# Kernel tuning notes

Measured on AMD Instinct MI355X. Metric: run time of the kernel, lower is better.

## Reference

```python
import jax, jax.numpy as jnp
import numpy as np

N_NODES = 50000
N_FEAT = 128
N_EDGES = 800000
HEADS1 = 4
HID1 = 64
HID2 = 128
N_CLASSES = 10
N_GRAPHS = 512
NEG_SLOPE_ATT = 0.2   # GATConv attention leaky relu
NEG_SLOPE_ACT = 0.01  # F.leaky_relu default between layers


def setup_inputs() -> dict:
    key = jax.random.key(0)
    ks = jax.random.split(key, 20)
    s = 0.05
    inp = {
        'x': jax.random.normal(ks[0], (N_NODES, N_FEAT), dtype=jnp.float32),
        'edge_index': jax.random.randint(ks[1], (2, N_EDGES), 0, N_NODES, dtype=jnp.int64),
        'edge_attr': jax.random.normal(ks[2], (N_EDGES, 8), dtype=jnp.float32),
        'batch': jnp.sort(jax.random.randint(ks[3], (N_NODES,), 0, N_GRAPHS, dtype=jnp.int64)),
        # conv1: F -> HID1, heads=4, concat
        'W1': jax.random.normal(ks[4], (N_FEAT, HEADS1 * HID1), dtype=jnp.float32) * s,
        'a_src1': jax.random.normal(ks[5], (HEADS1, HID1), dtype=jnp.float32) * s,
        'a_dst1': jax.random.normal(ks[6], (HEADS1, HID1), dtype=jnp.float32) * s,
        'b1': jnp.zeros((HEADS1 * HID1,), dtype=jnp.float32),
        # conv2: 4*HID1 -> HID2, heads=1
        'W2': jax.random.normal(ks[7], (HEADS1 * HID1, HID2), dtype=jnp.float32) * s,
        'a_src2': jax.random.normal(ks[8], (1, HID2), dtype=jnp.float32) * s,
        'a_dst2': jax.random.normal(ks[9], (1, HID2), dtype=jnp.float32) * s,
        'b2': jnp.zeros((HID2,), dtype=jnp.float32),
        # conv3: HID2 -> N_CLASSES, heads=1
        'W3': jax.random.normal(ks[10], (HID2, N_CLASSES), dtype=jnp.float32) * s,
        'a_src3': jax.random.normal(ks[11], (1, N_CLASSES), dtype=jnp.float32) * s,
        'a_dst3': jax.random.normal(ks[12], (1, N_CLASSES), dtype=jnp.float32) * s,
        'b3': jnp.zeros((N_CLASSES,), dtype=jnp.float32),
    }
    return inp


def gat_conv(x, src, dst, W, a_src, a_dst, b, n_nodes, heads, ch):
    """PyG GATConv (concat=True, add_self_loops already applied in src/dst)."""
    h = (x @ W).reshape(n_nodes, heads, ch)            # [N,H,C]
    al_s = (h * a_src).sum(-1)                          # [N,H]
    al_d = (h * a_dst).sum(-1)                          # [N,H]
    e = jax.nn.leaky_relu(al_s[src] + al_d[dst], NEG_SLOPE_ATT)  # [E,H]
    # segment softmax over incoming edges per destination node
    m = jax.ops.segment_max(e, dst, num_segments=n_nodes)
    ex = jnp.exp(e - m[dst])
    den = jax.ops.segment_sum(ex, dst, num_segments=n_nodes)
    alpha = ex / (den[dst] + 1e-16)                     # [E,H]
    out = jax.ops.segment_sum(h[src] * alpha[..., None], dst, num_segments=n_nodes)
    return out.reshape(n_nodes, heads * ch) + b


def reference(x, edge_index, edge_attr, batch,
              W1, a_src1, a_dst1, b1,
              W2, a_src2, a_dst2, b2,
              W3, a_src3, a_dst3, b3):
    # GATConv adds self-loops by default; edge_attr unused (edge_dim=None)
    loops = jnp.arange(N_NODES, dtype=edge_index.dtype)
    src = jnp.concatenate([edge_index[0], loops])
    dst = jnp.concatenate([edge_index[1], loops])

    h = gat_conv(x, src, dst, W1, a_src1, a_dst1, b1, N_NODES, HEADS1, HID1)
    h = jax.nn.leaky_relu(h, NEG_SLOPE_ACT)
    h = gat_conv(h, src, dst, W2, a_src2, a_dst2, b2, N_NODES, 1, HID2)
    h = jax.nn.leaky_relu(h, NEG_SLOPE_ACT)
    h = gat_conv(h, src, dst, W3, a_src3, a_dst3, b3, N_NODES, 1, N_CLASSES)

    pooled = jax.ops.segment_sum(h, batch, num_segments=N_GRAPHS)  # global_add_pool
    return jax.nn.log_softmax(pooled, axis=1), pooled
```

## Files before the change

kernel.cpp:

```cpp
#include <hip/hip_runtime.h>
#include <math.h>

#define NNODES 50000
#define MPAD   50048
#define NFEAT  128
#define NEDGE  800000
#define ETOT   (NEDGE + NNODES)
#define H1     4
#define O1     256
#define C2     128
#define C3     10
#define NGRAPH 512

#define NBKT   196
#define NBLK1  831
#define EPB    1024
#define SCM    (NBKT * NBLK1)
#define SCB    637

typedef __attribute__((ext_vector_type(8))) short short8;
typedef __attribute__((ext_vector_type(4))) float f32x4;
typedef __attribute__((ext_vector_type(2))) float f32x2;

__device__ __forceinline__ unsigned short f2b(float f) {
  unsigned int u = __float_as_uint(f);
  u += 0x7fffu + ((u >> 16) & 1u);
  return (unsigned short)(u >> 16);
}
__device__ __forceinline__ float b2f(unsigned short u) {
  return __uint_as_float(((unsigned int)u) << 16);
}
__device__ __forceinline__ float readlane_f(float v, int l) {
  return __uint_as_float((unsigned)__builtin_amdgcn_readlane(__float_as_uint(v), l));
}


__global__ void k_prep(const float* __restrict__ W1, const float* __restrict__ as1,
                       const float* __restrict__ ad1,
                       float* __restrict__ was, float* __restrict__ wad) {
  int tid = threadIdx.x;
  int h = tid >> 7, k = tid & 127;
  float s = 0.f, d = 0.f;
  for (int j = 0; j < 64; ++j) {
    float w = W1[(size_t)k * 256 + h * 64 + j];
    s += w * as1[h * 64 + j];
    d += w * ad1[h * 64 + j];
  }
  was[h * 128 + k] = s;
  wad[h * 128 + k] = d;
}

#define NB_CVT 12500

__global__ __launch_bounds__(256) void k_front(
    const int* __restrict__ src_e, const int* __restrict__ dst_e,
    int* __restrict__ hists,
    const float* __restrict__ X, unsigned short* __restrict__ Xb,
    const float* __restrict__ W1,
    const float* __restrict__ was, const float* __restrict__ wad,
    float* __restrict__ als, float* __restrict__ ald,
    unsigned short* __restrict__ W1p,
    const float* __restrict__ W2, unsigned short* __restrict__ W2p,
    const float* __restrict__ W3, unsigned short* __restrict__ W3p) {
  const int b = blockIdx.x;
  const int tid = threadIdx.x;
  if (b < NBLK1) {
    __shared__ int h[NBKT];
    if (tid < NBKT) h[tid] = 0;
    __syncthreads();
    const int base = b * EPB;
#pragma unroll
    for (int r = 0; r < 4; ++r) {
      int e = base + r * 256 + tid;
      if (e < ETOT) {
        int d = (e < NEDGE) ? dst_e[e] : (e - NEDGE);
        atomicAdd(&h[d >> 8], 1);
      }
    }
    __syncthreads();
    if (tid < NBKT) hists[tid * NBLK1 + b] = h[tid];
  } else if (b < NBLK1 + NB_CVT) {
    const int n = (b - NBLK1) * 4 + (tid >> 6);
    const int lane = tid & 63;
    const int k0 = lane * 2;
    float2 xv = *(const float2*)(X + (size_t)n * 128 + k0);
    ushort2 o; o.x = f2b(xv.x); o.y = f2b(xv.y);
    *(ushort2*)(Xb + (size_t)n * 128 + k0) = o;
    float s[4], d[4];
#pragma unroll
    for (int h = 0; h < 4; ++h) {
      float2 wsv = *(const float2*)(was + h * 128 + k0);
      float2 wdv = *(const float2*)(wad + h * 128 + k0);
      s[h] = xv.x * wsv.x + xv.y * wsv.y;
      d[h] = xv.x * wdv.x + xv.y * wdv.y;
    }
#pragma unroll
    for (int m = 1; m < 64; m <<= 1)
#pragma unroll
      for (int h = 0; h < 4; ++h) { s[h] += __shfl_xor(s[h], m); d[h] += __shfl_xor(d[h], m); }
    if (lane == 0) {
#pragma unroll
      for (int h = 0; h < 4; ++h) {
        als[(size_t)n * 4 + h] = s[h];
        ald[(size_t)n * 4 + h] = d[h];
      }
    }
  } else if (b < NBLK1 + NB_CVT + 128) {
    int idx = (b - NBLK1 - NB_CVT) * 256 + tid;
    int h = idx >> 13, r = idx & 8191;
    int j = r & 7, lane = (r >> 3) & 63, t = r >> 9;
    int ks = t & 3, nt = t >> 2;
    int k = ks * 32 + (lane >> 4) * 8 + j;
    int n = nt * 16 + (lane & 15);
    W1p[idx] = f2b(W1[(size_t)k * 256 + h * 64 + n]);
  } else if (b < NBLK1 + NB_CVT + 256) {
    int idx = (b - NBLK1 - NB_CVT - 128) * 256 + tid;
    int j = idx & 7, lane = (idx >> 3) & 63, t = idx >> 9;
    int ks = t % 8, nt = t / 8;
    int k = ks * 32 + (lane >> 4) * 8 + j;
    int n = nt * 16 + (lane & 15);
    W2p[idx] = f2b(W2[(size_t)k * C2 + n]);
  } else {
    int idx = (b - NBLK1 - NB_CVT - 256) * 256 + tid;
    int j = idx & 7, lane = (idx >> 3) & 63, t = idx >> 9;
    int ks = t & 3, nt = t >> 2;
    int k = ks * 32 + (lane >> 4) * 8 + j;
    int n = nt * 16 + (lane & 15);
    W3p[idx] = f2b((n < C3) ? W3[(size_t)k * C3 + n] : 0.f);
  }
}


__global__ __launch_bounds__(256) void k_scanA2(const int* __restrict__ a,
                                                int* __restrict__ bsum) {
  int idx = blockIdx.x * 256 + threadIdx.x;
  int v = (idx < SCM) ? a[idx] : 0;
#pragma unroll
  for (int m = 1; m < 64; m <<= 1) v += __shfl_xor(v, m);
  __shared__ int ws[4];
  int lane = threadIdx.x & 63, wid = threadIdx.x >> 6;
  if (lane == 0) ws[wid] = v;
  __syncthreads();
  if (threadIdx.x == 0) bsum[blockIdx.x] = ws[0] + ws[1] + ws[2] + ws[3];
}

__global__ __launch_bounds__(256) void k_scanMid(int* __restrict__ bsum) {
  __shared__ int ws[4];
  __shared__ int carry_s;
  const int tid = threadIdx.x, lane = tid & 63, wid = tid >> 6;
  if (tid == 0) carry_s = 0;
  __syncthreads();
  for (int base = 0; base < SCB; base += 256) {
    int j = base + tid;
    int v = (j < SCB) ? bsum[j] : 0;
    int s = v;
#pragma unroll
    for (int m = 1; m < 64; m <<= 1) {
      int t = __shfl_up(s, m);
      if (lane >= m) s += t;
    }
    if (lane == 63) ws[wid] = s;
    __syncthreads();
    int woff = 0;
#pragma unroll
    for (int k = 0; k < 4; ++k)
      if (k < wid) woff += ws[k];
    int c = carry_s;
    int tot = ws[0] + ws[1] + ws[2] + ws[3];
    if (j < SCB) bsum[j] = c + woff + s - v;
    __syncthreads();
    if (tid == 0) carry_s = c + tot;
    __syncthreads();
  }
}

__global__ __launch_bounds__(256) void k_scanB2(int* __restrict__ a,
                                                const int* __restrict__ bsum,
                                                int* __restrict__ cb) {
  const int b = blockIdx.x, tid = threadIdx.x;
  const int lane = tid & 63, wid = tid >> 6;
  __shared__ int ws[4];
  int idx = b * 256 + tid;
  int v = (idx < SCM) ? a[idx] : 0;
  int s = v;
#pragma unroll
  for (int m = 1; m < 64; m <<= 1) {
    int t = __shfl_up(s, m);
    if (lane >= m) s += t;
  }
  if (lane == 63) ws[wid] = s;
  __syncthreads();
  int woff = 0;
#pragma unroll
  for (int k = 0; k < 4; ++k)
    if (k < wid) woff += ws[k];
  int excl = bsum[b] + woff + s - v;
  if (idx < SCM) {
    a[idx] = excl;
    if (idx % NBLK1 == 0) cb[idx / NBLK1] = excl;
  }
  if (b == 0 && tid == 0) cb[NBKT] = ETOT;
}


__global__ __launch_bounds__(256) void k_part1(const int* __restrict__ src_e,
                                               const int* __restrict__ dst_e,
                                               const int* __restrict__ offs,
                                               unsigned* __restrict__ coarse) {
  __shared__ int cur[NBKT];
  const int b = blockIdx.x;
  const int tid = threadIdx.x;
  if (tid < NBKT) cur[tid] = offs[tid * NBLK1 + b];
  __syncthreads();
  const int base = b * EPB;
#pragma unroll
  for (int r = 0; r < 4; ++r) {
    int e = base + r * 256 + tid;
    if (e < ETOT) {
      int d, s;
      if (e < NEDGE) { d = dst_e[e]; s = src_e[e]; }
      else           { d = e - NEDGE; s = e - NEDGE; }
      int pos = atomicAdd(&cur[d >> 8], 1);
      coarse[pos] = ((unsigned)d << 16) | (unsigned)s;
    }
  }
}


__global__ __launch_bounds__(256) void k_bucket(const unsigned* __restrict__ coarse,
                                                const int* __restrict__ cb,
                                                int* __restrict__ rowptr,
                                                int* __restrict__ srcs) {
  const int b = blockIdx.x;
  const int tid = threadIdx.x;
  const int lane = tid & 63, wid = tid >> 6;
  const int lo = cb[b], hi = cb[b + 1];
  __shared__ int h[256];
  __shared__ int cur[256];
  __shared__ int ws[4];
  h[tid] = 0;
  __syncthreads();
  for (int i = lo + tid; i < hi; i += 256)
    atomicAdd(&h[(coarse[i] >> 16) & 255], 1);
  __syncthreads();
  int v = h[tid];
  int s = v;
#pragma unroll
  for (int m = 1; m < 64; m <<= 1) {
    int t = __shfl_up(s, m);
    if (lane >= m) s += t;
  }
  if (lane == 63) ws[wid] = s;
  __syncthreads();
  int woff = 0;
#pragma unroll
  for (int k = 0; k < 4; ++k)
    if (k < wid) woff += ws[k];
  int ex = woff + s - v;
  cur[tid] = lo + ex;
  int d = b * 256 + tid;
  if (d < NNODES) rowptr[d] = lo + ex;
  if (b == NBKT - 1 && tid == 0) rowptr[NNODES] = ETOT;
  __syncthreads();
  for (int i = lo + tid; i < hi; i += 256) {
    unsigned c = coarse[i];
    int pos = atomicAdd(&cur[(c >> 16) & 255], 1);
    srcs[pos] = (int)(c & 0xffffu);
  }
}


__global__ __launch_bounds__(512) void k_aggP(const int* __restrict__ rowptr,
                                              const int* __restrict__ srcs,
                                              const unsigned short* __restrict__ Xb,
                                              const float* __restrict__ als,
                                              const float* __restrict__ ald,
                                              unsigned short* __restrict__ P) {
  __shared__ float exs[8][16][4];
  const int wv = threadIdx.x >> 6;
  const int n = blockIdx.x * 8 + wv;
  const int lane = threadIdx.x & 63;
  const int r0 = rowptr[n], r1 = rowptr[n + 1];
  const int e_lane = lane & 15, hh = lane >> 4;
  const float aldv = ald[(size_t)n * 4 + hh];
  const int ch0 = lane * 2;
  f32x2 ah0 = {0.f, 0.f}, ah1 = {0.f, 0.f}, ah2 = {0.f, 0.f}, ah3 = {0.f, 0.f};
  float den = 0.f;
  for (int i0 = r0; i0 < r1; i0 += 16) {
    const int take = r1 - i0;
    int sidx = srcs[min(i0 + e_lane, r1 - 1)];
    float ev = als[(size_t)sidx * 4 + hh] + aldv;
    ev = (ev > 0.f) ? ev : 0.2f * ev;
    float exv = (e_lane < take) ? __expf(ev) : 0.f;
    den += exv;
    exs[wv][e_lane][hh] = exv;
    unsigned hv[16];
#pragma unroll
    for (int m = 0; m < 16; ++m) {
      int s = __builtin_amdgcn_readlane(sidx, m);
      hv[m] = *(const unsigned*)(Xb + (size_t)s * 128 + ch0);
    }
#pragma unroll
    for (int m = 0; m < 16; ++m) {
      f32x2 e01 = *(const f32x2*)(&exs[wv][m][0]);
      f32x2 e23 = *(const f32x2*)(&exs[wv][m][2]);
      f32x2 x2;
      x2.x = __uint_as_float(hv[m] << 16);
      x2.y = __uint_as_float(hv[m] & 0xffff0000u);
      asm("v_pk_fma_f32 %0, %1, %2, %0 op_sel:[0,0,0] op_sel_hi:[1,0,1]"
          : "+v"(ah0) : "v"(x2), "v"(e01));
      asm("v_pk_fma_f32 %0, %1, %2, %0 op_sel:[0,1,0] op_sel_hi:[1,1,1]"
          : "+v"(ah1) : "v"(x2), "v"(e01));
      asm("v_pk_fma_f32 %0, %1, %2, %0 op_sel:[0,0,0] op_sel_hi:[1,0,1]"
          : "+v"(ah2) : "v"(x2), "v"(e23));
      asm("v_pk_fma_f32 %0, %1, %2, %0 op_sel:[0,1,0] op_sel_hi:[1,1,1]"
          : "+v"(ah3) : "v"(x2), "v"(e23));
    }
  }
#pragma unroll
  for (int m = 1; m < 16; m <<= 1) den += __shfl_xor(den, m);
  float acc[4][2] = {{ah0.x, ah0.y}, {ah1.x, ah1.y}, {ah2.x, ah2.y}, {ah3.x, ah3.y}};
#pragma unroll
  for (int h = 0; h < 4; ++h) {
    float rd = 1.f / (readlane_f(den, h * 16) + 1e-16f);
    ushort2 o; o.x = f2b(acc[h][0] * rd); o.y = f2b(acc[h][1] * rd);
    *(ushort2*)(P + ((size_t)n * 4 + h) * 128 + ch0) = o;
  }
}


__global__ __launch_bounds__(256) void k_mmh(const unsigned short* __restrict__ P,
                                             const unsigned short* __restrict__ Wp,
                                             const float* __restrict__ b1,
                                             unsigned short* __restrict__ act1) {
  const int hy = blockIdx.y;
  const int w = threadIdx.x >> 6, lane = threadIdx.x & 63;
  const int arow = blockIdx.x * 64 + w * 16 + (lane & 15);
  const int k0 = (lane >> 4) * 8;
  const unsigned short* Ab = P + ((size_t)arow * 4 + hy) * 128;
  f32x4 acc[4] = {};
#pragma unroll
  for (int ks = 0; ks < 4; ++ks) {
    short8 a = *(const short8*)(Ab + ks * 32 + k0);
    const short8* bp = (const short8*)(Wp + (size_t)hy * 8192) + ks * 64 + lane;
#pragma unroll
    for (int nt = 0; nt < 4; ++nt) {
      short8 b = bp[(size_t)nt * 4 * 64];
      acc[nt] = __builtin_amdgcn_mfma_f32_16x16x32_bf16(a, b, acc[nt], 0, 0, 0);
    }
  }
  const int col = lane & 15;
  const int rbase = blockIdx.x * 64 + w * 16 + (lane >> 4) * 4;
#pragma unroll
  for (int nt = 0; nt < 4; ++nt) {
    int ch = hy * 64 + nt * 16 + col;
    float bb = b1[ch];
#pragma unroll
    for (int j = 0; j < 4; ++j) {
      float v = acc[nt][j] + bb;
      v = (v > 0.f) ? v : 0.01f * v;
      act1[(size_t)(rbase + j) * 256 + ch] = f2b(v);
    }
  }
}


template<int K, int N, int HEADS, int CREAL>
__global__ __launch_bounds__(256) void k_mm(const unsigned short* __restrict__ Xb,
                                            const unsigned short* __restrict__ Wp,
                                            unsigned short* __restrict__ Hout,
                                            const float* __restrict__ a_src,
                                            const float* __restrict__ a_dst,
                                            float* __restrict__ als,
                                            float* __restrict__ ald) {
  constexpr int KS = K / 32, NT = N / 16;
  constexpr int NTH = (NT + HEADS - 1) / HEADS;
  const int w = threadIdx.x >> 6, lane = threadIdx.x & 63;
  const int arow = blockIdx.x * 64 + w * 16 + (lane & 15);
  const int k0 = (lane >> 4) * 8;
  f32x4 acc[NT] = {};
  for (int ks = 0; ks < KS; ++ks) {
    short8 a = *(const short8*)(Xb + (size_t)arow * K + ks * 32 + k0);
    const short8* bp = (const short8*)Wp + (size_t)ks * 64 + lane;
#pragma unroll
    for (int nt = 0; nt < NT; ++nt) {
      short8 b = bp[(size_t)nt * KS * 64];
      acc[nt] = __builtin_amdgcn_mfma_f32_16x16x32_bf16(a, b, acc[nt], 0, 0, 0);
    }
  }
  const int col = lane & 15;
  const int rbase = blockIdx.x * 64 + w * 16 + (lane >> 4) * 4;
#pragma unroll
  for (int nt = 0; nt < NT; ++nt)
#pragma unroll
    for (int j = 0; j < 4; ++j)
      Hout[(size_t)(rbase + j) * N + nt * 16 + col] = f2b(acc[nt][j]);

  float av[NT], dv[NT];
#pragma unroll
  for (int nt = 0; nt < NT; ++nt) {
    int ch = nt * 16 + col;
    av[nt] = (ch < CREAL) ? a_src[ch] : 0.f;
    dv[nt] = (ch < CREAL) ? a_dst[ch] : 0.f;
  }
  float sa[HEADS][4], da[HEADS][4];
#pragma unroll
  for (int h = 0; h < HEADS; ++h)
#pragma unroll
    for (int j = 0; j < 4; ++j) { sa[h][j] = 0.f; da[h][j] = 0.f; }
#pragma unroll
  for (int nt = 0; nt < NT; ++nt) {
    int h = nt / NTH;
#pragma unroll
    for (int j = 0; j < 4; ++j) {
      sa[h][j] += acc[nt][j] * av[nt];
      da[h][j] += acc[nt][j] * dv[nt];
    }
  }
#pragma unroll
  for (int mask = 1; mask < 16; mask <<= 1)
#pragma unroll
    for (int h = 0; h < HEADS; ++h)
#pragma unroll
      for (int j = 0; j < 4; ++j) {
        sa[h][j] += __shfl_xor(sa[h][j], mask);
        da[h][j] += __shfl_xor(da[h][j], mask);
      }
  if (col == 0) {
#pragma unroll
    for (int j = 0; j < 4; ++j)
#pragma unroll
      for (int h = 0; h < HEADS; ++h) {
        als[(size_t)(rbase + j) * HEADS + h] = sa[h][j];
        ald[(size_t)(rbase + j) * HEADS + h] = da[h][j];
      }
  }
}


template<int C, bool ACT>
__global__ __launch_bounds__(512) void k_agg(const int* __restrict__ rowptr,
                                             const int* __restrict__ srcs,
                                             const unsigned short* __restrict__ Hm,
                                             const float* __restrict__ als,
                                             const float* __restrict__ ald,
                                             const float* __restrict__ bias,
                                             unsigned short* __restrict__ outb) {
  __shared__ float exs2[8][16];
  const int wv = threadIdx.x >> 6;
  const int n = blockIdx.x * 8 + wv;
  const int lane = threadIdx.x & 63;
  const int r0 = rowptr[n], r1 = rowptr[n + 1];
  const int e_lane = lane & 15;
  const int ch0 = lane * 2;
  const float aldm = ald[n];
  f32x2 accP0 = {0.f, 0.f}, accP1 = {0.f, 0.f};
  float den = 0.f;
  for (int i0 = r0; i0 < r1; i0 += 16) {
    const int take = r1 - i0;
    int sidx = srcs[min(i0 + e_lane, r1 - 1)];
    float ev = als[sidx] + aldm;
    ev = (ev > 0.f) ? ev : 0.2f * ev;
    float exv = (lane < 16 && e_lane < take) ? __expf(ev) : 0.f;
    den += exv;
    if (lane < 16) exs2[wv][lane] = exv;
    unsigned hv[16];
#pragma unroll
    for (int m = 0; m < 16; ++m) {
      int s = __builtin_amdgcn_readlane(sidx, m);
      hv[m] = *(const unsigned*)(Hm + (size_t)s * C + ch0);
    }
#pragma unroll
    for (int m = 0; m < 16; m += 2) {
      f32x2 ep = *(const f32x2*)(&exs2[wv][m]);
      f32x2 xa, xb;
      xa.x = __uint_as_float(hv[m] << 16);
      xa.y = __uint_as_float(hv[m + 1] << 16);
      xb.x = __uint_as_float(hv[m] & 0xffff0000u);
      xb.y = __uint_as_float(hv[m + 1] & 0xffff0000u);
      asm("v_pk_fma_f32 %0, %1, %2, %0" : "+v"(accP0) : "v"(ep), "v"(xa));
      asm("v_pk_fma_f32 %0, %1, %2, %0" : "+v"(accP1) : "v"(ep), "v"(xb));
    }
  }
#pragma unroll
  for (int mask = 1; mask < 64; mask <<= 1) den += __shfl_xor(den, mask);
  float acc0 = accP0.x + accP0.y;
  float acc1 = accP1.x + accP1.y;
  float rden = 1.f / (den + 1e-16f);
  float v0 = acc0 * rden + bias[ch0];
  float v1 = acc1 * rden + bias[ch0 + 1];
  if (ACT) { v0 = (v0 > 0.f) ? v0 : 0.01f * v0; v1 = (v1 > 0.f) ? v1 : 0.01f * v1; }
  ushort2 o; o.x = f2b(v0); o.y = f2b(v1);
  *(ushort2*)(outb + (size_t)n * C + ch0) = o;
}


__global__ __launch_bounds__(512) void k_agg3(const int* __restrict__ rowptr,
                                              const int* __restrict__ srcs,
                                              const unsigned short* __restrict__ Hm,
                                              const float* __restrict__ als,
                                              const float* __restrict__ ald,
                                              const float* __restrict__ bias,
                                              float* __restrict__ pooled,
                                              const int* __restrict__ batch) {
  __shared__ int   sid_s[8][4][16];
  __shared__ float exv_s[8][4][16];
  const int wv = threadIdx.x >> 6;
  const int lane = threadIdx.x & 63;
  const int g = lane >> 4, el = lane & 15;
  const int n = blockIdx.x * 32 + wv * 4 + g;
  const bool valid = n < NNODES;
  int r0 = 0, r1 = 0;
  float aldm = 0.f;
  if (valid) { r0 = rowptr[n]; r1 = rowptr[n + 1]; aldm = ald[n]; }
  float acc = 0.f, den = 0.f;
  for (int i0 = r0; i0 < r1; i0 += 16) {
    const int take = r1 - i0;
    int sidx = srcs[min(i0 + el, r1 - 1)];
    float ev = als[sidx] + aldm;
    ev = (ev > 0.f) ? ev : 0.2f * ev;
    float exv = (el < take) ? __expf(ev) : 0.f;
    den += exv;
    sid_s[wv][g][el] = sidx;
    exv_s[wv][g][el] = exv;
#pragma unroll
    for (int m = 0; m < 16; ++m) {
      int s = sid_s[wv][g][m];
      float ex = exv_s[wv][g][m];
      acc += ex * b2f(Hm[(size_t)s * 16 + el]);
    }
  }
#pragma unroll
  for (int mask = 1; mask < 16; mask <<= 1) den += __shfl_xor(den, mask);
  if (valid && el < C3) {
    float val = acc / (den + 1e-16f) + bias[el];
    atomicAdd(&pooled[(size_t)batch[n] * C3 + el], val);
  }
}


__global__ void k_lsm(const float* __restrict__ pooled, float* __restrict__ dout) {
  int g = blockIdx.x * 256 + threadIdx.x;
  if (g >= NGRAPH) return;
  float v[C3];
  float mx = -1e30f;
#pragma unroll
  for (int c = 0; c < C3; ++c) { v[c] = pooled[g * C3 + c]; mx = fmaxf(mx, v[c]); }
  float ssum = 0.f;
#pragma unroll
  for (int c = 0; c < C3; ++c) ssum += __expf(v[c] - mx);
  float lse = mx + __logf(ssum);
#pragma unroll
  for (int c = 0; c < C3; ++c) {
    dout[g * C3 + c] = v[c] - lse;
    dout[NGRAPH * C3 + g * C3 + c] = v[c];
  }
}


extern "C" void kernel_launch(void* const* d_in, const int* in_sizes, int n_in,
                              void* d_out, int out_size, void* d_ws, size_t ws_size,
                              hipStream_t stream) {
  (void)in_sizes; (void)n_in; (void)out_size; (void)ws_size;
  const float* x     = (const float*)d_in[0];
  const int*   eix   = (const int*)d_in[1];
  const int*   batch = (const int*)d_in[3];
  const float* W1 = (const float*)d_in[4];
  const float* as1 = (const float*)d_in[5];
  const float* ad1 = (const float*)d_in[6];
  const float* b1 = (const float*)d_in[7];
  const float* W2 = (const float*)d_in[8];
  const float* as2 = (const float*)d_in[9];
  const float* ad2 = (const float*)d_in[10];
  const float* b2 = (const float*)d_in[11];
  const float* W3 = (const float*)d_in[12];
  const float* as3 = (const float*)d_in[13];
  const float* ad3 = (const float*)d_in[14];
  const float* b3 = (const float*)d_in[15];
  const int* src_e = eix;
  const int* dst_e = eix + NEDGE;

  char* ws = (char*)d_ws;
  size_t off = 0;
  auto carve = [&](size_t bytes) -> char* {
    char* p = ws + off;
    off += (bytes + 511) & ~(size_t)511;
    return p;
  };
  int* hists  = (int*)carve((size_t)SCM * 4);
  int* bsum   = (int*)carve((size_t)SCB * 4);
  int* cb     = (int*)carve((size_t)(NBKT + 1) * 4);
  unsigned* coarse = (unsigned*)carve((size_t)ETOT * 4);
  int* rowptr = (int*)carve((size_t)(NNODES + 1) * 4);
  int* srcs   = (int*)carve((size_t)ETOT * 4);
  float* als  = (float*)carve((size_t)MPAD * H1 * 4);
  float* ald  = (float*)carve((size_t)MPAD * H1 * 4);
  float* was  = (float*)carve((size_t)512 * 4);
  float* wad  = (float*)carve((size_t)512 * 4);
  unsigned short* Xb   = (unsigned short*)carve((size_t)MPAD * 128 * 2);
  unsigned short* P    = (unsigned short*)carve((size_t)MPAD * 512 * 2);
  unsigned short* act1 = (unsigned short*)carve((size_t)MPAD * 256 * 2);
  unsigned short* Hb   = (unsigned short*)carve((size_t)MPAD * 128 * 2);
  unsigned short* Xc   = (unsigned short*)carve((size_t)MPAD * 128 * 2);
  unsigned short* H3b  = (unsigned short*)carve((size_t)MPAD * 16 * 2);
  float* pooled = (float*)carve((size_t)NGRAPH * C3 * 4);
  unsigned short* W1p = (unsigned short*)carve((size_t)4 * 8192 * 2);
  unsigned short* W2p = (unsigned short*)carve((size_t)O1 * C2 * 2);
  unsigned short* W3p = (unsigned short*)carve((size_t)C2 * 16 * 2);

  hipMemsetAsync(pooled, 0, (size_t)NGRAPH * C3 * 4, stream);

  k_prep<<<1, 512, 0, stream>>>(W1, as1, ad1, was, wad);
  k_front<<<NBLK1 + NB_CVT + 264, 256, 0, stream>>>(
      src_e, dst_e, hists, x, Xb, W1, was, wad, als, ald, W1p, W2, W2p, W3, W3p);
  k_scanA2<<<SCB, 256, 0, stream>>>(hists, bsum);
  k_scanMid<<<1, 256, 0, stream>>>(bsum);
  k_scanB2<<<SCB, 256, 0, stream>>>(hists, bsum, cb);
  k_part1<<<NBLK1, 256, 0, stream>>>(src_e, dst_e, hists, coarse);
  k_bucket<<<NBKT, 256, 0, stream>>>(coarse, cb, rowptr, srcs);

  const int GB = MPAD / 64;
  const int NB8 = NNODES / 8;
  const int NB32 = (NNODES + 31) / 32;

  k_aggP<<<NB8, 512, 0, stream>>>(rowptr, srcs, Xb, als, ald, P);
  k_mmh<<<dim3(GB, 4), 256, 0, stream>>>(P, W1p, b1, act1);

  k_mm<O1, C2, 1, C2><<<GB, 256, 0, stream>>>(act1, W2p, Hb, as2, ad2, als, ald);
  k_agg<C2, true><<<NB8, 512, 0, stream>>>(rowptr, srcs, Hb, als, ald, b2, Xc);

  k_mm<C2, 16, 1, C3><<<GB, 256, 0, stream>>>(Xc, W3p, H3b, as3, ad3, als, ald);
  k_agg3<<<NB32, 512, 0, stream>>>(rowptr, srcs, H3b, als, ald, b3, pooled, batch);

  k_lsm<<<(NGRAPH + 255) / 256, 256, 0, stream>>>(pooled, (float*)d_out);
}
```

Measured before the change: 226.4 us.

## Fuse layer-1 head matmul into aggP and layer-3 matmul into layer-2 aggregation

Layer-1 aggregation now keeps the per-node aggregated head features in shared memory and runs the per-head projection with MFMA inside the same block. This removes the large P intermediate buffer and the separate k_mmh launch. Layer-2 aggregation likewise stages its activated output in LDS and computes the conv3 projection and attention logits in one wave, so the Xc buffer and a k_mm launch go away. The cost is extra block-wide syncs, MFMA tiles that are half wasted (8 of 16 rows valid), and idle waves during the fused matmul.

```diff
diff --git a/kernel.cpp b/kernel.cpp
--- a/kernel.cpp
+++ b/kernel.cpp
@@ -275,8 +275,11 @@
                                               const unsigned short* __restrict__ Xb,
                                               const float* __restrict__ als,
                                               const float* __restrict__ ald,
-                                              unsigned short* __restrict__ P) {
+                                              const unsigned short* __restrict__ W1p,
+                                              const float* __restrict__ b1,
+                                              unsigned short* __restrict__ act1) {
   __shared__ float exs[8][16][4];
+  __shared__ unsigned short Pl[8][4][128];
   const int wv = threadIdx.x >> 6;
   const int n = blockIdx.x * 8 + wv;
   const int lane = threadIdx.x & 63;
@@ -324,42 +327,36 @@
   for (int h = 0; h < 4; ++h) {
     float rd = 1.f / (readlane_f(den, h * 16) + 1e-16f);
     ushort2 o; o.x = f2b(acc[h][0] * rd); o.y = f2b(acc[h][1] * rd);
-    *(ushort2*)(P + ((size_t)n * 4 + h) * 128 + ch0) = o;
-  }
-}
-
-
-__global__ __launch_bounds__(256) void k_mmh(const unsigned short* __restrict__ P,
-                                             const unsigned short* __restrict__ Wp,
-                                             const float* __restrict__ b1,
-                                             unsigned short* __restrict__ act1) {
-  const int hy = blockIdx.y;
-  const int w = threadIdx.x >> 6, lane = threadIdx.x & 63;
-  const int arow = blockIdx.x * 64 + w * 16 + (lane & 15);
+    *(ushort2*)(&Pl[wv][h][ch0]) = o;
+  }
+  __syncthreads();
+
+  const int row = lane & 15;
   const int k0 = (lane >> 4) * 8;
-  const unsigned short* Ab = P + ((size_t)arow * 4 + hy) * 128;
-  f32x4 acc[4] = {};
-#pragma unroll
-  for (int ks = 0; ks < 4; ++ks) {
-    short8 a = *(const short8*)(Ab + ks * 32 + k0);
-    const short8* bp = (const short8*)(Wp + (size_t)hy * 8192) + ks * 64 + lane;
-#pragma unroll
-    for (int nt = 0; nt < 4; ++nt) {
-      short8 b = bp[(size_t)nt * 4 * 64];
-      acc[nt] = __builtin_amdgcn_mfma_f32_16x16x32_bf16(a, b, acc[nt], 0, 0, 0);
-    }
-  }
   const int col = lane & 15;
-  const int rbase = blockIdx.x * 64 + w * 16 + (lane >> 4) * 4;
-#pragma unroll
-  for (int nt = 0; nt < 4; ++nt) {
-    int ch = hy * 64 + nt * 16 + col;
-    float bb = b1[ch];
+  const int rb = (lane >> 4) * 4;
+#pragma unroll
+  for (int u = 0; u < 2; ++u) {
+    const int unit = wv + 8 * u;
+    const int h = unit >> 2, nt = unit & 3;
+    f32x4 acc2 = {};
+#pragma unroll
+    for (int ks = 0; ks < 4; ++ks) {
+      short8 a{};
+      if (row < 8) a = *(const short8*)(&Pl[row][h][ks * 32 + k0]);
+      short8 b = *((const short8*)(W1p + (size_t)h * 8192) + nt * 256 + ks * 64 + lane);
+      acc2 = __builtin_amdgcn_mfma_f32_16x16x32_bf16(a, b, acc2, 0, 0, 0);
+    }
+    const int ch = h * 64 + nt * 16 + col;
+    const float bb = b1[ch];
 #pragma unroll
     for (int j = 0; j < 4; ++j) {
-      float v = acc[nt][j] + bb;
-      v = (v > 0.f) ? v : 0.01f * v;
-      act1[(size_t)(rbase + j) * 256 + ch] = f2b(v);
+      int r = rb + j;
+      if (r < 8) {
+        float v = acc2[j] + bb;
+        v = (v > 0.f) ? v : 0.01f * v;
+        act1[(size_t)(blockIdx.x * 8 + r) * 256 + ch] = f2b(v);
+      }
     }
   }
 }
@@ -438,15 +435,20 @@
 }
 
 
-template<int C, bool ACT>
-__global__ __launch_bounds__(512) void k_agg(const int* __restrict__ rowptr,
-                                             const int* __restrict__ srcs,
-                                             const unsigned short* __restrict__ Hm,
-                                             const float* __restrict__ als,
-                                             const float* __restrict__ ald,
-                                             const float* __restrict__ bias,
-                                             unsigned short* __restrict__ outb) {
+__global__ __launch_bounds__(512) void k_agg2(const int* __restrict__ rowptr,
+                                              const int* __restrict__ srcs,
+                                              const unsigned short* __restrict__ Hm,
+                                              const float* __restrict__ als,
+                                              const float* __restrict__ ald,
+                                              const float* __restrict__ bias,
+                                              const unsigned short* __restrict__ W3p,
+                                              const float* __restrict__ as3,
+                                              const float* __restrict__ ad3,
+                                              unsigned short* __restrict__ H3b,
+                                              float* __restrict__ als3,
+                                              float* __restrict__ ald3) {
   __shared__ float exs2[8][16];
+  __shared__ unsigned short Xl[8][128];
   const int wv = threadIdx.x >> 6;
   const int n = blockIdx.x * 8 + wv;
   const int lane = threadIdx.x & 63;
@@ -468,7 +470,7 @@
 #pragma unroll
     for (int m = 0; m < 16; ++m) {
       int s = __builtin_amdgcn_readlane(sidx, m);
-      hv[m] = *(const unsigned*)(Hm + (size_t)s * C + ch0);
+      hv[m] = *(const unsigned*)(Hm + (size_t)s * C2 + ch0);
     }
 #pragma unroll
     for (int m = 0; m < 16; m += 2) {
@@ -484,14 +486,47 @@
   }
 #pragma unroll
   for (int mask = 1; mask < 64; mask <<= 1) den += __shfl_xor(den, mask);
-  float acc0 = accP0.x + accP0.y;
-  float acc1 = accP1.x + accP1.y;
   float rden = 1.f / (den + 1e-16f);
-  float v0 = acc0 * rden + bias[ch0];
-  float v1 = acc1 * rden + bias[ch0 + 1];
-  if (ACT) { v0 = (v0 > 0.f) ? v0 : 0.01f * v0; v1 = (v1 > 0.f) ? v1 : 0.01f * v1; }
+  float v0 = (accP0.x + accP0.y) * rden + bias[ch0];
+  float v1 = (accP1.x + accP1.y) * rden + bias[ch0 + 1];
+  v0 = (v0 > 0.f) ? v0 : 0.01f * v0;
+  v1 = (v1 > 0.f) ? v1 : 0.01f * v1;
   ushort2 o; o.x = f2b(v0); o.y = f2b(v1);
-  *(ushort2*)(outb + (size_t)n * C + ch0) = o;
+  *(ushort2*)(&Xl[wv][ch0]) = o;
+  __syncthreads();
+
+  if (wv == 0) {
+    const int row = lane & 15;
+    const int k0 = (lane >> 4) * 8;
+    const int col = lane & 15;
+    f32x4 acc2 = {};
+#pragma unroll
+    for (int ks = 0; ks < 4; ++ks) {
+      short8 a{};
+      if (row < 8) a = *(const short8*)(&Xl[row][ks * 32 + k0]);
+      short8 b = *((const short8*)W3p + ks * 64 + lane);
+      acc2 = __builtin_amdgcn_mfma_f32_16x16x32_bf16(a, b, acc2, 0, 0, 0);
+    }
+    const float av = (col < C3) ? as3[col] : 0.f;
+    const float dv = (col < C3) ? ad3[col] : 0.f;
+    const int rb = (lane >> 4) * 4;
+#pragma unroll
+    for (int j = 0; j < 4; ++j) {
+      float hv = acc2[j];
+      float sa = hv * av, da = hv * dv;
+#pragma unroll
+      for (int mask = 1; mask < 16; mask <<= 1) {
+        sa += __shfl_xor(sa, mask);
+        da += __shfl_xor(da, mask);
+      }
+      int r = rb + j;
+      if (r < 8) {
+        int node = blockIdx.x * 8 + r;
+        H3b[(size_t)node * 16 + col] = f2b(hv);
+        if (col == 0) { als3[node] = sa; ald3[node] = da; }
+      }
+    }
+  }
 }
 
 
@@ -595,13 +630,13 @@
   int* srcs   = (int*)carve((size_t)ETOT * 4);
   float* als  = (float*)carve((size_t)MPAD * H1 * 4);
   float* ald  = (float*)carve((size_t)MPAD * H1 * 4);
+  float* als3 = (float*)carve((size_t)MPAD * 4);
+  float* ald3 = (float*)carve((size_t)MPAD * 4);
   float* was  = (float*)carve((size_t)512 * 4);
   float* wad  = (float*)carve((size_t)512 * 4);
   unsigned short* Xb   = (unsigned short*)carve((size_t)MPAD * 128 * 2);
-  unsigned short* P    = (unsigned short*)carve((size_t)MPAD * 512 * 2);
   unsigned short* act1 = (unsigned short*)carve((size_t)MPAD * 256 * 2);
   unsigned short* Hb   = (unsigned short*)carve((size_t)MPAD * 128 * 2);
-  unsigned short* Xc   = (unsigned short*)carve((size_t)MPAD * 128 * 2);
   unsigned short* H3b  = (unsigned short*)carve((size_t)MPAD * 16 * 2);
   float* pooled = (float*)carve((size_t)NGRAPH * C3 * 4);
   unsigned short* W1p = (unsigned short*)carve((size_t)4 * 8192 * 2);
@@ -623,14 +658,13 @@
   const int NB8 = NNODES / 8;
   const int NB32 = (NNODES + 31) / 32;
 
-  k_aggP<<<NB8, 512, 0, stream>>>(rowptr, srcs, Xb, als, ald, P);
-  k_mmh<<<dim3(GB, 4), 256, 0, stream>>>(P, W1p, b1, act1);
+  k_aggP<<<NB8, 512, 0, stream>>>(rowptr, srcs, Xb, als, ald, W1p, b1, act1);
 
   k_mm<O1, C2, 1, C2><<<GB, 256, 0, stream>>>(act1, W2p, Hb, as2, ad2, als, ald);
-  k_agg<C2, true><<<NB8, 512, 0, stream>>>(rowptr, srcs, Hb, als, ald, b2, Xc);
-
-  k_mm<C2, 16, 1, C3><<<GB, 256, 0, stream>>>(Xc, W3p, H3b, as3, ad3, als, ald);
-  k_agg3<<<NB32, 512, 0, stream>>>(rowptr, srcs, H3b, als, ald, b3, pooled, batch);
+  k_agg2<<<NB8, 512, 0, stream>>>(rowptr, srcs, Hb, als, ald, b2,
+                                  W3p, as3, ad3, H3b, als3, ald3);
+
+  k_agg3<<<NB32, 512, 0, stream>>>(rowptr, srcs, H3b, als3, ald3, b3, pooled, batch);
 
   k_lsm<<<(NGRAPH + 255) / 256, 256, 0, stream>>>(pooled, (float*)d_out);
 }
```

Result: no change. 227.5 us (+0.5%).
